# Optimization experiments

Hardware: AMD Instinct MI355X
Metric: run time of the kernel (lower is better)

Reference implementation:

```python
import jax, jax.numpy as jnp
import numpy as np
import math

B, S, D, H, FF = 2, 2048, 1024, 16, 4096
HD = D // H
EPS = 1e-5


def setup_inputs() -> dict:
    key = jax.random.key(0)
    ks = jax.random.split(key, 16)
    w = lambda k, shape: (jax.random.normal(k, shape, jnp.float32) * 0.02)
    future = jnp.triu(jnp.ones((S, S), dtype=bool), k=1)
    causal_mask = jnp.where(future, -jnp.inf, 0.0).astype(jnp.float32)
    return {
        "src": jax.random.normal(ks[0], (B, S, D), jnp.float32),
        "causal_mask": causal_mask,
        "Wq": w(ks[1], (D, D)), "bq": jnp.zeros((D,), jnp.float32),
        "Wk": w(ks[2], (D, D)), "bk": jnp.zeros((D,), jnp.float32),
        "Wv": w(ks[3], (D, D)), "bv": jnp.zeros((D,), jnp.float32),
        "Wo": w(ks[4], (D, D)), "bo": jnp.zeros((D,), jnp.float32),
        "W1": w(ks[5], (D, FF)), "b1": jnp.zeros((FF,), jnp.float32),
        "W2": w(ks[6], (FF, D)), "b2": jnp.zeros((D,), jnp.float32),
        "ln1_g": jnp.ones((D,), jnp.float32), "ln1_b": jnp.zeros((D,), jnp.float32),
        "ln2_g": jnp.ones((D,), jnp.float32), "ln2_b": jnp.zeros((D,), jnp.float32),
    }


def _layernorm(x, g, b):
    mu = jnp.mean(x, axis=-1, keepdims=True)
    var = jnp.mean((x - mu) ** 2, axis=-1, keepdims=True)
    return (x - mu) * jax.lax.rsqrt(var + EPS) * g + b


def reference(src, causal_mask, Wq, bq, Wk, bk, Wv, bv, Wo, bo,
              W1, b1, W2, b2, ln1_g, ln1_b, ln2_g, ln2_b):
    # QKV projections, split heads: [B,S,D] -> [B,H,S,HD]
    def split_heads(x):
        return x.reshape(B, S, H, HD).transpose(0, 2, 1, 3)

    q = split_heads(src @ Wq + bq)
    k = split_heads(src @ Wk + bk)
    v = split_heads(src @ Wv + bv)

    # scores: [B,H,S,S]; attn_mask = causal_mask broadcast over batch, then head dim
    scores = jnp.einsum("bhqd,bhkd->bhqk", q, k) / math.sqrt(HD)
    scores = scores + causal_mask[None, None, :, :]
    # scores[scores != scores] = 0
    scores = jnp.where(jnp.isnan(scores), 0.0, scores)
    # rows that are entirely inf -> 0
    mask_all_inf = jnp.all(jnp.isinf(scores), axis=-1, keepdims=True)
    scores = jnp.where(mask_all_inf, 0.0, scores)
    attn = jax.nn.softmax(scores, axis=-1)
    attn = jnp.where(jnp.isnan(attn), 0.0, attn)

    ctx = jnp.einsum("bhqk,bhkd->bhqd", attn, v)
    ctx = ctx.transpose(0, 2, 1, 3).reshape(B, S, D)
    attn_out = ctx @ Wo + bo

    x = _layernorm(src + attn_out, ln1_g, ln1_b)
    ff = jax.nn.relu(x @ W1 + b1) @ W2 + b2
    return _layernorm(x + ff, ln2_g, ln2_b)
```

## Files before the change

### kernel.cpp

```cpp
#include <hip/hip_runtime.h>

#define SS 2048
#define DD 1024
#define HH 16
#define HDIM 64
#define BB 2
#define FFD 4096
#define MR (BB*SS)
#define QKVLD 3072

typedef __bf16 bf16;
typedef __bf16 bf16x4 __attribute__((ext_vector_type(4)));
typedef __bf16 bf16x8 __attribute__((ext_vector_type(8)));
typedef float f32x4 __attribute__((ext_vector_type(4)));

struct P4 { bf16* p[4]; };
struct TP4 { const float* src[4]; bf16* dst[4]; float scale[4]; };

__device__ inline f32x4 mfma32(bf16x8 a, bf16x8 b, f32x4 c) {
  return __builtin_amdgcn_mfma_f32_16x16x32_bf16(a, b, c, 0, 0, 0);
}

__device__ inline void gload_lds16(const void* g, void* l) {
  __builtin_amdgcn_global_load_lds(
      (const __attribute__((address_space(1))) void*)g,
      (__attribute__((address_space(3))) void*)l, 16, 0, 0);
}

#if defined(__has_builtin)
#if __has_builtin(__builtin_amdgcn_exp2f)
#define HAVE_EXP2_BUILTIN 1
#endif
#endif
__device__ inline float fast_exp2(float x) {
#ifdef HAVE_EXP2_BUILTIN
  return __builtin_amdgcn_exp2f(x);
#else
  float r; asm("v_exp_f32 %0, %1" : "=v"(r) : "v"(x)); return r;
#endif
}

__global__ __launch_bounds__(256)
void cvt_bf16_kernel(const float* __restrict__ in, bf16* __restrict__ out, int n) {
  int i = (blockIdx.x * 256 + threadIdx.x) * 4;
  if (i >= n) return;
  float4 v = *(const float4*)(in + i);
  bf16x4 o;
  o[0] = (bf16)v.x; o[1] = (bf16)v.y; o[2] = (bf16)v.z; o[3] = (bf16)v.w;
  *(bf16x4*)(out + i) = o;
}

__global__ __launch_bounds__(256)
void concat_bias_kernel(const float* __restrict__ bq, const float* __restrict__ bk,
                        const float* __restrict__ bv, float* __restrict__ out) {
  int i = blockIdx.x * 256 + threadIdx.x;
  const float K2 = 0.18033688f;
  out[i] = i < 1024 ? bq[i] * K2 : (i < 2048 ? bk[i - 1024] : bv[i - 2048]);
}

__global__ __launch_bounds__(256)
void transpose_w4_kernel(TP4 t) {
  __shared__ float tl[32][33];
  const float* W = t.src[blockIdx.z];
  bf16* Wt = t.dst[blockIdx.z];
  const float sc = t.scale[blockIdx.z];
  int tx = threadIdx.x & 31, ty = threadIdx.x >> 5;
  int n0 = blockIdx.x * 32, k0 = blockIdx.y * 32;
  #pragma unroll
  for (int i = 0; i < 4; ++i)
    tl[ty + i*8][tx] = W[(size_t)(k0 + ty + i*8) * DD + n0 + tx];
  __syncthreads();
  #pragma unroll
  for (int i = 0; i < 4; ++i)
    Wt[(size_t)(n0 + ty + i*8) * DD + k0 + tx] = (bf16)(tl[tx][ty + i*8] * sc);
}

__global__ __launch_bounds__(256)
void transpose_w_kernel(const float* __restrict__ W, bf16* __restrict__ Wt,
                        int K, int N) {
  __shared__ float t[32][33];
  int tx = threadIdx.x & 31, ty = threadIdx.x >> 5;
  int n0 = blockIdx.x * 32, k0 = blockIdx.y * 32;
  #pragma unroll
  for (int i = 0; i < 4; ++i)
    t[ty + i*8][tx] = W[(size_t)(k0 + ty + i*8) * N + n0 + tx];
  __syncthreads();
  #pragma unroll
  for (int i = 0; i < 4; ++i)
    Wt[(size_t)(n0 + ty + i*8) * K + k0 + tx] = (bf16)t[tx][ty + i*8];
}

__global__ __launch_bounds__(256)
void transpose_v_kernel(const bf16* __restrict__ V2d, bf16* __restrict__ Vt) {
  __shared__ bf16 t[32][33];
  int tx = threadIdx.x & 31, ty = threadIdx.x >> 5;
  int s0 = blockIdx.x * 32, d0 = blockIdx.y * 32;
  int bh = blockIdx.z;
  int b = bh >> 4, h = bh & 15;
  #pragma unroll
  for (int i = 0; i < 4; ++i)
    t[ty + i*8][tx] = V2d[(size_t)(b*SS + s0 + ty + i*8) * QKVLD + h*HDIM + d0 + tx];
  __syncthreads();
  #pragma unroll
  for (int i = 0; i < 4; ++i)
    Vt[((size_t)bh*HDIM + d0 + ty + i*8) * SS + s0 + tx] = t[tx][ty + i*8];
}

template<int OUT_BF16, int RELU, int SPLITK>
__global__ __launch_bounds__(512)
void gemm_h(const bf16* __restrict__ A, const bf16* __restrict__ Bt,
            const float* __restrict__ bias, void* __restrict__ Cout,
            P4 part, int Ndim, int Kdim) {
  __shared__ bf16 Asm[2][128 * 32];
  __shared__ bf16 Bsm[2][256 * 32];
  const int gx = gridDim.x, gy = gridDim.y;
  const int gxy = gx * gy;
  const int nwg = gxy * gridDim.z;
  const int lin = (blockIdx.z * gy + blockIdx.y) * gx + blockIdx.x;
  const int swz = (lin & 7) * (nwg >> 3) + (lin >> 3);
  int bz = 0, rem = swz;
  if (SPLITK > 1) { bz = swz / gxy; rem = swz - bz * gxy; }
  const int by = rem / gx, bx = rem - by * gx;
  const int m0 = by * 128, n0 = bx * 256;
  const int tid = threadIdx.x;
  const int wave = tid >> 6, lane = tid & 63;
  const int g = lane >> 4, r = lane & 15;
  const int wr = wave >> 2, wn = wave & 3;
  const int kstart = bz * (Kdim / SPLITK);

  const int lrow = lane >> 2;
  const int lslot = (lane & 3) ^ (lrow & 3);
  const bf16* Ag = A + (size_t)(m0 + wave * 16 + lrow) * Kdim + kstart + lslot * 8;
  const bf16* Bg0 = Bt + (size_t)(n0 + wave * 32 + lrow) * Kdim + kstart + lslot * 8;
  const bf16* Bg1 = Bg0 + (size_t)16 * Kdim;

  f32x4 acc[4][4] = {};
  const int NT = (Kdim / SPLITK) >> 5;

  auto stage = [&](int t) {
    const int kb = t << 5;
    bf16* Ad = Asm[t & 1] + wave * 512;
    bf16* Bd = Bsm[t & 1] + wave * 1024;
    gload_lds16(Ag + kb, Ad);
    gload_lds16(Bg0 + kb, Bd);
    gload_lds16(Bg1 + kb, Bd + 512);
  };

  stage(0);
  __syncthreads();

  for (int t = 0; t < NT; ++t) {
    const bf16* Ab = Asm[t & 1];
    const bf16* Bb = Bsm[t & 1];
    bf16x8 af[4], bfr[4];
    #pragma unroll
    for (int i = 0; i < 4; ++i) {
      const int row = wr * 64 + i * 16 + r;
      af[i] = *(const bf16x8*)(Ab + row * 32 + ((g ^ (r & 3)) * 8));
    }
    #pragma unroll
    for (int i = 0; i < 4; ++i) {
      const int rowb = wn * 64 + i * 16 + r;
      bfr[i] = *(const bf16x8*)(Bb + rowb * 32 + ((g ^ (r & 3)) * 8));
    }
    if (t + 1 < NT) stage(t + 1);
    __builtin_amdgcn_s_setprio(1);
    #pragma unroll
    for (int i = 0; i < 4; ++i)
      #pragma unroll
      for (int jn = 0; jn < 4; ++jn)
        acc[i][jn] = mfma32(af[i], bfr[jn], acc[i][jn]);
    __builtin_amdgcn_s_setprio(0);
    __syncthreads();
  }

  #pragma unroll
  for (int mi = 0; mi < 4; ++mi) {
    #pragma unroll
    for (int ni = 0; ni < 4; ++ni) {
      const int col = n0 + wn * 64 + ni * 16 + r;
      const float bv = (SPLITK > 1) ? 0.f : bias[col];
      #pragma unroll
      for (int jj = 0; jj < 4; ++jj) {
        const int row = m0 + wr * 64 + mi * 16 + g * 4 + jj;
        float v = acc[mi][ni][jj] + bv;
        if (RELU) v = fmaxf(v, 0.f);
        if (SPLITK > 1) part.p[bz][(size_t)row * Ndim + col] = (bf16)v;
        else if (OUT_BF16) ((bf16*)Cout)[(size_t)row * Ndim + col] = (bf16)v;
        else               ((float*)Cout)[(size_t)row * Ndim + col] = v;
      }
    }
  }
}

__global__ __launch_bounds__(256)
void attn_kernel(const bf16* __restrict__ Q2d, const bf16* __restrict__ K2d,
                 const bf16* __restrict__ Vt, bf16* __restrict__ ctx) {
  __shared__ bf16 Ks[2 * 4096];
  __shared__ bf16 Vs[2 * 4096];
  const int tid = threadIdx.x;
  const int wave = tid >> 6;
  const int lane = tid & 63;
  const int g = lane >> 4, r = lane & 15;
  const int lin = blockIdx.y * gridDim.x + blockIdx.x;
  const int swz = (lin & 7) * 64 + (lin >> 3);
  const int p = swz & 15;
  const int bh = swz >> 4;
  const int b = bh >> 4, h = bh & 15;

  const int strow = wave * 16 + (lane >> 2);
  const int lslot = (lane & 3) ^ ((lane >> 3) & 3);
  const bf16* srcK0 = K2d + (size_t)(b*SS + strow) * QKVLD + h*HDIM + lslot * 8;
  const bf16* srcK1 = srcK0 + 32;
  const bf16* srcV0 = Vt + ((size_t)bh*HDIM + strow) * SS + lslot * 8;
  const bf16* srcV1 = srcV0 + 32;

  auto sw = [](int row, int s) { return row * 32 + ((s ^ ((row >> 1) & 3)) * 8); };

  const int kr0 = 8 * (r >> 2) + (r & 3);
  const int oKa0 = sw(kr0,      g), oKb0 = 2048 + oKa0;
  const int oKa1 = sw(kr0 +  4, g), oKb1 = 2048 + oKa1;
  const int oKa2 = sw(kr0 + 32, g), oKb2 = 2048 + oKa2;
  const int oKa3 = sw(kr0 + 36, g), oKb3 = 2048 + oKa3;
  int oV[4];
  #pragma unroll
  for (int c = 0; c < 4; ++c) oV[c] = sw(c * 16 + r, g);

  bf16x8 onesf;
  #pragma unroll
  for (int j = 0; j < 8; ++j) onesf[j] = (bf16)1.0f;

  #pragma unroll
  for (int tt = 0; tt < 2; ++tt) {
    const int tile = tt ? (31 - p) : p;
    const int q0 = tile * 64 + wave * 16;
    const int qg = q0 + r;
    const bf16* qp = Q2d + (size_t)(b*SS + q0 + r) * QKVLD + h * HDIM;
    const bf16x8 qf0 = *(const bf16x8*)(qp + g * 8);
    const bf16x8 qf1 = *(const bf16x8*)(qp + 32 + g * 8);
    f32x4 ov[4] = {};
    f32x4 lacc = {};
    const int nst = tile + 1;
    {
      bf16* kb = Ks + wave * 512;
      bf16* vb = Vs + wave * 512;
      gload_lds16(srcK0, kb);
      gload_lds16(srcK1, kb + 2048);
      gload_lds16(srcV0, vb);
      gload_lds16(srcV1, vb + 2048);
    }
    __syncthreads();
    int cur = 0;
    for (int st = 0; st < nst; ++st) {
      const int k0 = st * 64;
      if (st + 1 < nst) {
        const int kn = k0 + 64;
        bf16* kb = Ks + (cur ^ 1) * 4096 + wave * 512;
        bf16* vb = Vs + (cur ^ 1) * 4096 + wave * 512;
        gload_lds16(srcK0 + (size_t)kn * QKVLD, kb);
        gload_lds16(srcK1 + (size_t)kn * QKVLD, kb + 2048);
        gload_lds16(srcV0 + kn, vb);
        gload_lds16(srcV1 + kn, vb + 2048);
      }
      const bf16* Kb = Ks + cur * 4096;
      const bf16* Vb = Vs + cur * 4096;
      f32x4 c0 = {}, c1 = {}, c2 = {}, c3 = {};
      __builtin_amdgcn_s_setprio(1);
      c0 = mfma32(*(const bf16x8*)(Kb + oKa0), qf0, c0);
      c1 = mfma32(*(const bf16x8*)(Kb + oKa1), qf0, c1);
      c2 = mfma32(*(const bf16x8*)(Kb + oKa2), qf0, c2);
      c3 = mfma32(*(const bf16x8*)(Kb + oKa3), qf0, c3);
      c0 = mfma32(*(const bf16x8*)(Kb + oKb0), qf1, c0);
      c1 = mfma32(*(const bf16x8*)(Kb + oKb1), qf1, c1);
      c2 = mfma32(*(const bf16x8*)(Kb + oKb2), qf1, c2);
      c3 = mfma32(*(const bf16x8*)(Kb + oKb3), qf1, c3);
      __builtin_amdgcn_s_setprio(0);
      float p0[4], p1[4], p2[4], p3[4];
      const bool need_mask = (k0 + 63 > qg);
      #pragma unroll
      for (int j = 0; j < 4; ++j) {
        float s0 = c0[j];
        float s1 = c1[j];
        float s2 = c2[j];
        float s3 = c3[j];
        if (need_mask) {
          if (k0 + 8*g + j > qg)          s0 = -3.0e38f;
          if (k0 + 8*g + 4 + j > qg)      s1 = -3.0e38f;
          if (k0 + 32 + 8*g + j > qg)     s2 = -3.0e38f;
          if (k0 + 32 + 8*g + 4 + j > qg) s3 = -3.0e38f;
        }
        p0[j] = fast_exp2(s0);
        p1[j] = fast_exp2(s1);
        p2[j] = fast_exp2(s2);
        p3[j] = fast_exp2(s3);
      }
      bf16x8 pfa, pfb;
      #pragma unroll
      for (int j = 0; j < 4; ++j) {
        pfa[j] = (bf16)p0[j]; pfa[4 + j] = (bf16)p1[j];
        pfb[j] = (bf16)p2[j]; pfb[4 + j] = (bf16)p3[j];
      }
      __builtin_amdgcn_s_setprio(1);
      #pragma unroll
      for (int c = 0; c < 4; ++c) {
        bf16x8 vfa = *(const bf16x8*)(Vb + oV[c]);
        bf16x8 vfb = *(const bf16x8*)(Vb + 2048 + oV[c]);
        ov[c] = mfma32(pfa, vfa, ov[c]);
        ov[c] = mfma32(pfb, vfb, ov[c]);
      }
      lacc = mfma32(pfa, onesf, lacc);
      lacc = mfma32(pfb, onesf, lacc);
      __builtin_amdgcn_s_setprio(0);
      __syncthreads();
      cur ^= 1;
    }
    #pragma unroll
    for (int j = 0; j < 4; ++j) {
      const float inv = 1.f / lacc[j];
      const int row = b*SS + q0 + 4*g + j;
      #pragma unroll
      for (int c = 0; c < 4; ++c)
        ctx[(size_t)row * DD + h*HDIM + c*16 + r] = (bf16)(ov[c][j] * inv);
    }
  }
}

template<int WRITEB>
__global__ __launch_bounds__(256)
void ln_bf4_kernel(const float* __restrict__ a, P4 part, const float* __restrict__ cb,
                   const float* __restrict__ gam, const float* __restrict__ bet,
                   float* __restrict__ outf, bf16* __restrict__ outb) {
  const int row = blockIdx.x;
  const int tid = threadIdx.x;
  const size_t base = (size_t)row * DD + tid * 4;
  float4 va = *(const float4*)(a + base);
  bf16x4 u0 = *(const bf16x4*)(part.p[0] + base);
  bf16x4 u1 = *(const bf16x4*)(part.p[1] + base);
  bf16x4 u2 = *(const bf16x4*)(part.p[2] + base);
  bf16x4 u3 = *(const bf16x4*)(part.p[3] + base);
  float4 vb4 = *(const float4*)(cb + tid * 4);
  float x0 = va.x + ((float)u0[0] + (float)u1[0]) + ((float)u2[0] + (float)u3[0]) + vb4.x;
  float x1 = va.y + ((float)u0[1] + (float)u1[1]) + ((float)u2[1] + (float)u3[1]) + vb4.y;
  float x2 = va.z + ((float)u0[2] + (float)u1[2]) + ((float)u2[2] + (float)u3[2]) + vb4.z;
  float x3 = va.w + ((float)u0[3] + (float)u1[3]) + ((float)u2[3] + (float)u3[3]) + vb4.w;
  float s  = x0 + x1 + x2 + x3;
  float s2 = x0*x0 + x1*x1 + x2*x2 + x3*x3;
  #pragma unroll
  for (int off = 32; off > 0; off >>= 1) {
    s  += __shfl_xor(s,  off);
    s2 += __shfl_xor(s2, off);
  }
  __shared__ float red[8];
  const int wv = tid >> 6;
  if ((tid & 63) == 0) { red[wv] = s; red[wv + 4] = s2; }
  __syncthreads();
  s  = red[0] + red[1] + red[2] + red[3];
  s2 = red[4] + red[5] + red[6] + red[7];
  const float mu  = s * (1.f / DD);
  const float var = s2 * (1.f / DD) - mu * mu;
  const float rs  = rsqrtf(var + 1e-5f);
  float4 vg = *(const float4*)(gam + tid * 4);
  float4 vb = *(const float4*)(bet + tid * 4);
  float y0 = (x0 - mu) * rs * vg.x + vb.x;
  float y1 = (x1 - mu) * rs * vg.y + vb.y;
  float y2 = (x2 - mu) * rs * vg.z + vb.z;
  float y3 = (x3 - mu) * rs * vg.w + vb.w;
  float4 yo; yo.x = y0; yo.y = y1; yo.z = y2; yo.w = y3;
  *(float4*)(outf + base) = yo;
  if (WRITEB) {
    bf16x4 ob;
    ob[0] = (bf16)y0; ob[1] = (bf16)y1; ob[2] = (bf16)y2; ob[3] = (bf16)y3;
    *(bf16x4*)(outb + base) = ob;
  }
}

extern "C" void kernel_launch(void* const* d_in, const int* in_sizes, int n_in,
                              void* d_out, int out_size, void* d_ws, size_t ws_size,
                              hipStream_t stream) {
  const float* src  = (const float*)d_in[0];
  const float* Wq   = (const float*)d_in[2];
  const float* bq   = (const float*)d_in[3];
  const float* Wk   = (const float*)d_in[4];
  const float* bk   = (const float*)d_in[5];
  const float* Wv   = (const float*)d_in[6];
  const float* bv   = (const float*)d_in[7];
  const float* Wo   = (const float*)d_in[8];
  const float* bo   = (const float*)d_in[9];
  const float* W1   = (const float*)d_in[10];
  const float* b1   = (const float*)d_in[11];
  const float* W2   = (const float*)d_in[12];
  const float* b2   = (const float*)d_in[13];
  const float* ln1g = (const float*)d_in[14];
  const float* ln1b = (const float*)d_in[15];
  const float* ln2g = (const float*)d_in[16];
  const float* ln2b = (const float*)d_in[17];

  char* ws = (char*)d_ws;
  const size_t MB = 1024 * 1024;
  bf16* wqkvt = (bf16*)(ws + 0 * MB);
  bf16* wot   = (bf16*)(ws + 6 * MB);
  bf16* w1t   = (bf16*)(ws + 8 * MB);
  bf16* w2t   = (bf16*)(ws + 16 * MB);
  bf16* bsrc  = (bf16*)(ws + 24 * MB);
  bf16* xb    = bsrc;
  bf16* qkv   = (bf16*)(ws + 32 * MB);
  bf16* vt    = (bf16*)(ws + 56 * MB);
  bf16* ctx   = (bf16*)(ws + 64 * MB);
  bf16* ff1   = qkv;
  float* xf   = (float*)(ws + 72 * MB);
  float* bqkv = (float*)(ws + 88 * MB);
  float* outp = (float*)d_out;

  P4 wop;
  wop.p[0] = (bf16*)(ws + 32 * MB);
  wop.p[1] = (bf16*)(ws + 40 * MB);
  wop.p[2] = (bf16*)(ws + 48 * MB);
  wop.p[3] = (bf16*)(ws + 56 * MB);
  P4 fp;
  fp.p[0] = (bf16*)(ws + 0 * MB);
  fp.p[1] = (bf16*)(ws + 8 * MB);
  fp.p[2] = (bf16*)(ws + 24 * MB);
  fp.p[3] = (bf16*)(ws + 64 * MB);

  cvt_bf16_kernel<<<(MR * DD) / 1024, 256, 0, stream>>>(src, bsrc, MR * DD);
  TP4 tp;
  tp.src[0] = Wq; tp.dst[0] = wqkvt;              tp.scale[0] = 0.18033688f;
  tp.src[1] = Wk; tp.dst[1] = wqkvt + 1024*1024;  tp.scale[1] = 1.f;
  tp.src[2] = Wv; tp.dst[2] = wqkvt + 2048*1024;  tp.scale[2] = 1.f;
  tp.src[3] = Wo; tp.dst[3] = wot;                tp.scale[3] = 1.f;
  transpose_w4_kernel<<<dim3(32, 32, 4), 256, 0, stream>>>(tp);
  transpose_w_kernel<<<dim3(128, 32), 256, 0, stream>>>(W1, w1t, DD, FFD);
  transpose_w_kernel<<<dim3(32, 128), 256, 0, stream>>>(W2, w2t, FFD, DD);
  concat_bias_kernel<<<12, 256, 0, stream>>>(bq, bk, bv, bqkv);

  gemm_h<1, 0, 1><<<dim3(QKVLD / 256, MR / 128), 512, 0, stream>>>(bsrc, wqkvt, bqkv, qkv, P4{}, QKVLD, DD);
  transpose_v_kernel<<<dim3(SS / 32, HDIM / 32, BB * HH), 256, 0, stream>>>(qkv + 2048, vt);

  attn_kernel<<<dim3(16, BB * HH), 256, 0, stream>>>(qkv, qkv + 1024, vt, ctx);

  gemm_h<0, 0, 4><<<dim3(DD / 256, MR / 128, 4), 512, 0, stream>>>(ctx, wot, nullptr, nullptr, wop, DD, DD);
  ln_bf4_kernel<1><<<MR, 256, 0, stream>>>(src, wop, bo, ln1g, ln1b, xf, xb);

  gemm_h<1, 1, 1><<<dim3(FFD / 256, MR / 128), 512, 0, stream>>>(xb, w1t, b1, ff1, P4{}, FFD, DD);
  gemm_h<0, 0, 4><<<dim3(DD / 256, MR / 128, 4), 512, 0, stream>>>(ff1, w2t, nullptr, nullptr, fp, DD, FFD);
  ln_bf4_kernel<0><<<MR, 256, 0, stream>>>(xf, fp, b2, ln2g, ln2b, outp, nullptr);
}
```

Before: 219.8 us.

## Widen attention KV tile to 128 keys and fix GEMM LDS swizzle

The attention kernel now stages 128 keys per iteration instead of 64, doubling the K and V LDS buffers and halving the number of loop iterations and barriers. This amortizes synchronization and load-issue overhead but raises LDS use and register pressure, and adds wasted work on the diagonal tile because masking now covers 128 keys. The GEMM LDS swizzle is changed to XOR with (row>>1)&3 on both the load and read sides, which is meant to cut bank conflicts on fragment reads. The wider tile also assumes causal tile counts divide evenly: for odd tiles, the last 128-key block extends past the diagonal, and correctness there relies on masking.

After: 214.2 us. 2.6% less time.

```diff
diff --git a/kernel.cpp b/kernel.cpp
--- a/kernel.cpp
+++ b/kernel.cpp
@@ -129,7 +129,7 @@
   const int kstart = bz * (Kdim / SPLITK);
 
   const int lrow = lane >> 2;
-  const int lslot = (lane & 3) ^ (lrow & 3);
+  const int lslot = (lane & 3) ^ ((lane >> 3) & 3);
   const bf16* Ag = A + (size_t)(m0 + wave * 16 + lrow) * Kdim + kstart + lslot * 8;
   const bf16* Bg0 = Bt + (size_t)(n0 + wave * 32 + lrow) * Kdim + kstart + lslot * 8;
   const bf16* Bg1 = Bg0 + (size_t)16 * Kdim;
@@ -149,6 +149,7 @@
   stage(0);
   __syncthreads();
 
+  const int rsw = (r >> 1) & 3;
   for (int t = 0; t < NT; ++t) {
     const bf16* Ab = Asm[t & 1];
     const bf16* Bb = Bsm[t & 1];
@@ -156,12 +157,12 @@
     #pragma unroll
     for (int i = 0; i < 4; ++i) {
       const int row = wr * 64 + i * 16 + r;
-      af[i] = *(const bf16x8*)(Ab + row * 32 + ((g ^ (r & 3)) * 8));
+      af[i] = *(const bf16x8*)(Ab + row * 32 + ((g ^ rsw) * 8));
     }
     #pragma unroll
     for (int i = 0; i < 4; ++i) {
       const int rowb = wn * 64 + i * 16 + r;
-      bfr[i] = *(const bf16x8*)(Bb + rowb * 32 + ((g ^ (r & 3)) * 8));
+      bfr[i] = *(const bf16x8*)(Bb + rowb * 32 + ((g ^ rsw) * 8));
     }
     if (t + 1 < NT) stage(t + 1);
     __builtin_amdgcn_s_setprio(1);
@@ -196,8 +197,8 @@
 __global__ __launch_bounds__(256)
 void attn_kernel(const bf16* __restrict__ Q2d, const bf16* __restrict__ K2d,
                  const bf16* __restrict__ Vt, bf16* __restrict__ ctx) {
-  __shared__ bf16 Ks[2 * 4096];
-  __shared__ bf16 Vs[2 * 4096];
+  __shared__ bf16 Ks[2 * 8192];
+  __shared__ bf16 Vs[2 * 8192];
   const int tid = threadIdx.x;
   const int wave = tid >> 6;
   const int lane = tid & 63;
@@ -210,10 +211,12 @@
 
   const int strow = wave * 16 + (lane >> 2);
   const int lslot = (lane & 3) ^ ((lane >> 3) & 3);
-  const bf16* srcK0 = K2d + (size_t)(b*SS + strow) * QKVLD + h*HDIM + lslot * 8;
-  const bf16* srcK1 = srcK0 + 32;
-  const bf16* srcV0 = Vt + ((size_t)bh*HDIM + strow) * SS + lslot * 8;
-  const bf16* srcV1 = srcV0 + 32;
+  const bf16* srcK0  = K2d + (size_t)(b*SS + strow) * QKVLD + h*HDIM + lslot * 8;
+  const bf16* srcK1  = srcK0 + 32;
+  const bf16* srcKh0 = srcK0 + (size_t)64 * QKVLD;
+  const bf16* srcKh1 = srcK1 + (size_t)64 * QKVLD;
+  const bf16* srcV0  = Vt + ((size_t)bh*HDIM + strow) * SS + lslot * 8;
+  const bf16* srcV1  = srcV0 + 32;
 
   auto sw = [](int row, int s) { return row * 32 + ((s ^ ((row >> 1) & 3)) * 8); };
 
@@ -240,31 +243,40 @@
     const bf16x8 qf1 = *(const bf16x8*)(qp + 32 + g * 8);
     f32x4 ov[4] = {};
     f32x4 lacc = {};
-    const int nst = tile + 1;
+    const int nst = (tile >> 1) + 1;
     {
       bf16* kb = Ks + wave * 512;
       bf16* vb = Vs + wave * 512;
-      gload_lds16(srcK0, kb);
-      gload_lds16(srcK1, kb + 2048);
-      gload_lds16(srcV0, vb);
-      gload_lds16(srcV1, vb + 2048);
+      gload_lds16(srcK0,  kb);
+      gload_lds16(srcK1,  kb + 2048);
+      gload_lds16(srcKh0, kb + 4096);
+      gload_lds16(srcKh1, kb + 6144);
+      gload_lds16(srcV0,      vb);
+      gload_lds16(srcV1,      vb + 2048);
+      gload_lds16(srcV0 + 64, vb + 4096);
+      gload_lds16(srcV1 + 64, vb + 6144);
     }
     __syncthreads();
     int cur = 0;
     for (int st = 0; st < nst; ++st) {
-      const int k0 = st * 64;
+      const int k0 = st * 128;
       if (st + 1 < nst) {
-        const int kn = k0 + 64;
-        bf16* kb = Ks + (cur ^ 1) * 4096 + wave * 512;
-        bf16* vb = Vs + (cur ^ 1) * 4096 + wave * 512;
-        gload_lds16(srcK0 + (size_t)kn * QKVLD, kb);
-        gload_lds16(srcK1 + (size_t)kn * QKVLD, kb + 2048);
-        gload_lds16(srcV0 + kn, vb);
-        gload_lds16(srcV1 + kn, vb + 2048);
+        const int kn = k0 + 128;
+        bf16* kb = Ks + (cur ^ 1) * 8192 + wave * 512;
+        bf16* vb = Vs + (cur ^ 1) * 8192 + wave * 512;
+        gload_lds16(srcK0  + (size_t)kn * QKVLD, kb);
+        gload_lds16(srcK1  + (size_t)kn * QKVLD, kb + 2048);
+        gload_lds16(srcKh0 + (size_t)kn * QKVLD, kb + 4096);
+        gload_lds16(srcKh1 + (size_t)kn * QKVLD, kb + 6144);
+        gload_lds16(srcV0 + kn,      vb);
+        gload_lds16(srcV1 + kn,      vb + 2048);
+        gload_lds16(srcV0 + kn + 64, vb + 4096);
+        gload_lds16(srcV1 + kn + 64, vb + 6144);
       }
-      const bf16* Kb = Ks + cur * 4096;
-      const bf16* Vb = Vs + cur * 4096;
+      const bf16* Kb = Ks + cur * 8192;
+      const bf16* Vb = Vs + cur * 8192;
       f32x4 c0 = {}, c1 = {}, c2 = {}, c3 = {};
+      f32x4 c4 = {}, c5 = {}, c6 = {}, c7 = {};
       __builtin_amdgcn_s_setprio(1);
       c0 = mfma32(*(const bf16x8*)(Kb + oKa0), qf0, c0);
       c1 = mfma32(*(const bf16x8*)(Kb + oKa1), qf0, c1);
@@ -274,42 +286,64 @@
       c1 = mfma32(*(const bf16x8*)(Kb + oKb1), qf1, c1);
       c2 = mfma32(*(const bf16x8*)(Kb + oKb2), qf1, c2);
       c3 = mfma32(*(const bf16x8*)(Kb + oKb3), qf1, c3);
+      c4 = mfma32(*(const bf16x8*)(Kb + 4096 + oKa0), qf0, c4);
+      c5 = mfma32(*(const bf16x8*)(Kb + 4096 + oKa1), qf0, c5);
+      c6 = mfma32(*(const bf16x8*)(Kb + 4096 + oKa2), qf0, c6);
+      c7 = mfma32(*(const bf16x8*)(Kb + 4096 + oKa3), qf0, c7);
+      c4 = mfma32(*(const bf16x8*)(Kb + 4096 + oKb0), qf1, c4);
+      c5 = mfma32(*(const bf16x8*)(Kb + 4096 + oKb1), qf1, c5);
+      c6 = mfma32(*(const bf16x8*)(Kb + 4096 + oKb2), qf1, c6);
+      c7 = mfma32(*(const bf16x8*)(Kb + 4096 + oKb3), qf1, c7);
       __builtin_amdgcn_s_setprio(0);
-      float p0[4], p1[4], p2[4], p3[4];
-      const bool need_mask = (k0 + 63 > qg);
+      float p0[4], p1[4], p2[4], p3[4], p4[4], p5[4], p6[4], p7[4];
+      const bool need_mask = (k0 + 127 > qg);
       #pragma unroll
       for (int j = 0; j < 4; ++j) {
-        float s0 = c0[j];
-        float s1 = c1[j];
-        float s2 = c2[j];
-        float s3 = c3[j];
+        float s0 = c0[j], s1 = c1[j], s2 = c2[j], s3 = c3[j];
+        float s4 = c4[j], s5 = c5[j], s6 = c6[j], s7 = c7[j];
         if (need_mask) {
-          if (k0 + 8*g + j > qg)          s0 = -3.0e38f;
-          if (k0 + 8*g + 4 + j > qg)      s1 = -3.0e38f;
-          if (k0 + 32 + 8*g + j > qg)     s2 = -3.0e38f;
-          if (k0 + 32 + 8*g + 4 + j > qg) s3 = -3.0e38f;
+          if (k0 + 8*g + j > qg)           s0 = -3.0e38f;
+          if (k0 + 8*g + 4 + j > qg)       s1 = -3.0e38f;
+          if (k0 + 32 + 8*g + j > qg)      s2 = -3.0e38f;
+          if (k0 + 32 + 8*g + 4 + j > qg)  s3 = -3.0e38f;
+          if (k0 + 64 + 8*g + j > qg)      s4 = -3.0e38f;
+          if (k0 + 64 + 8*g + 4 + j > qg)  s5 = -3.0e38f;
+          if (k0 + 96 + 8*g + j > qg)      s6 = -3.0e38f;
+          if (k0 + 96 + 8*g + 4 + j > qg)  s7 = -3.0e38f;
         }
         p0[j] = fast_exp2(s0);
         p1[j] = fast_exp2(s1);
         p2[j] = fast_exp2(s2);
         p3[j] = fast_exp2(s3);
+        p4[j] = fast_exp2(s4);
+        p5[j] = fast_exp2(s5);
+        p6[j] = fast_exp2(s6);
+        p7[j] = fast_exp2(s7);
       }
-      bf16x8 pfa, pfb;
+      bf16x8 pfa, pfb, pfc, pfd;
       #pragma unroll
       for (int j = 0; j < 4; ++j) {
         pfa[j] = (bf16)p0[j]; pfa[4 + j] = (bf16)p1[j];
         pfb[j] = (bf16)p2[j]; pfb[4 + j] = (bf16)p3[j];
+        pfc[j] = (bf16)p4[j]; pfc[4 + j] = (bf16)p5[j];
+        pfd[j] = (bf16)p6[j]; pfd[4 + j] = (bf16)p7[j];
       }
       __builtin_amdgcn_s_setprio(1);
       #pragma unroll
       for (int c = 0; c < 4; ++c) {
         bf16x8 vfa = *(const bf16x8*)(Vb + oV[c]);
         bf16x8 vfb = *(const bf16x8*)(Vb + 2048 + oV[c]);
+        bf16x8 vfc = *(const bf16x8*)(Vb + 4096 + oV[c]);
+        bf16x8 vfd = *(const bf16x8*)(Vb + 6144 + oV[c]);
         ov[c] = mfma32(pfa, vfa, ov[c]);
         ov[c] = mfma32(pfb, vfb, ov[c]);
+        ov[c] = mfma32(pfc, vfc, ov[c]);
+        ov[c] = mfma32(pfd, vfd, ov[c]);
       }
       lacc = mfma32(pfa, onesf, lacc);
       lacc = mfma32(pfb, onesf, lacc);
+      lacc = mfma32(pfc, onesf, lacc);
+      lacc = mfma32(pfd, onesf, lacc);
       __builtin_amdgcn_s_setprio(0);
       __syncthreads();
       cur ^= 1;
```
